# Kernel tuning notes

Measured on AMD Instinct MI355X. Metric: run time of the kernel, lower is better.

Reference implementation:

```python
import jax, jax.numpy as jnp
import numpy as np

HEADS = 16

def setup_inputs() -> dict:
    key = jax.random.key(0)
    k0, k1, k2, k3 = jax.random.split(key, 4)
    B, L, D = 2, 2048, 2048
    q = jax.random.normal(k0, (B, L, D), dtype=jnp.float32)
    k = jax.random.normal(k1, (B, L, D), dtype=jnp.float32)
    v = jax.random.normal(k2, (B, L, D), dtype=jnp.float32)
    wo = jax.random.normal(k3, (D, D), dtype=jnp.float32) * (1.0 / np.sqrt(D))
    return {"q": q, "k": k, "v": v, "wo": wo}

def reference(q, k, v, wo):
    B, Lq, D = q.shape
    Lk = k.shape[1]
    H = HEADS
    hd = D // H
    # [B, L, D] -> [B, H, L, hd]
    qh = q.reshape(B, Lq, H, hd).transpose(0, 2, 1, 3)
    kh = k.reshape(B, Lk, H, hd).transpose(0, 2, 1, 3)
    vh = v.reshape(B, Lk, H, hd).transpose(0, 2, 1, 3)
    scale = 1.0 / np.sqrt(hd).astype(np.float32)
    scores = jnp.einsum('bhqd,bhkd->bhqk', qh, kh) * scale
    cache_len = Lk - Lq
    # additive causal mask: -10000 above diagonal offset cache_len+1
    mask = jnp.triu(jnp.full((Lq, Lk), -10000.0, dtype=scores.dtype), k=cache_len + 1)
    attn = jax.nn.softmax(scores + mask, axis=-1)  # dropout p=0.0 => identity
    out = jnp.einsum('bhqk,bhkd->bhqd', attn, vh)
    out = out.transpose(0, 2, 1, 3).reshape(B, Lq, D)
    out = out @ wo.T  # torch Linear: x @ W^T
    return (out, kh, vh)
```

## Files before the change

kernel.cpp:

```cpp
#include <hip/hip_runtime.h>


typedef __attribute__((ext_vector_type(8))) __bf16 bf16x8;
typedef __attribute__((ext_vector_type(4))) float f32x4;
typedef __attribute__((ext_vector_type(4))) unsigned int uint32x4;

__device__ __forceinline__ unsigned short f2bf(float f) {
  union { float f; unsigned int u; } v; v.f = f;
  return (unsigned short)((v.u + 0x7FFFu + ((v.u >> 16) & 1u)) >> 16);
}
__device__ __forceinline__ __bf16 tobf(float f) {
  unsigned short u = f2bf(f);
  __bf16 r;
  __builtin_memcpy(&r, &u, 2);
  return r;
}
__device__ __forceinline__ float bfval(unsigned short u) {
  return __builtin_bit_cast(float, ((unsigned int)u) << 16);
}
__device__ __forceinline__ f32x4 zero4() {
  f32x4 z = {0.0f, 0.0f, 0.0f, 0.0f};
  return z;
}
__device__ __forceinline__ void gld_lds16(const unsigned short* g, unsigned short* l) {
  __builtin_amdgcn_global_load_lds(
      (const __attribute__((address_space(1))) unsigned int*)g,
      (__attribute__((address_space(3))) unsigned int*)l, 16, 0, 0);
}

__global__ __launch_bounds__(256) void conv_k(const float* __restrict__ k,
                                              float* __restrict__ kh,
                                              unsigned short* __restrict__ kbf) {
  int t = blockIdx.x * 256 + threadIdx.x;
  int d4 = t & 31;
  int l  = (t >> 5) & 2047;
  int h  = (t >> 16) & 15;
  int b  = t >> 20;
  const float4 v = *(const float4*)(k + ((size_t)(b * 2048 + l)) * 2048 + h * 128 + d4 * 4);
  size_t dst = (size_t)t * 4;
  *(float4*)(kh + dst) = v;
  *(ushort4*)(kbf + dst) = make_ushort4(f2bf(v.x), f2bf(v.y), f2bf(v.z), f2bf(v.w));
}

__global__ __launch_bounds__(256) void conv_wo(const float* __restrict__ wo,
                                               unsigned short* __restrict__ wobf) {
  int t = blockIdx.x * 256 + threadIdx.x;
  size_t dst = (size_t)t * 4;
  const float4 v = *(const float4*)(wo + dst);
  *(ushort4*)(wobf + dst) = make_ushort4(f2bf(v.x), f2bf(v.y), f2bf(v.z), f2bf(v.w));
}

__global__ __launch_bounds__(256) void conv_v(const float* __restrict__ v,
                                              float* __restrict__ vh,
                                              unsigned short* __restrict__ vbt) {
  __shared__ __align__(16) unsigned short T[128 * 72];
  const int tid = threadIdx.x;
  const int bid = blockIdx.x;
  const int lt = bid & 31;
  const int h  = (bid >> 5) & 15;
  const int b  = bid >> 9;
  const int l0 = lt * 64;
  const int bh = b * 16 + h;
#pragma unroll
  for (int i = 0; i < 8; ++i) {
    int c = tid + 256 * i;
    int row = c >> 5, col4 = c & 31;
    const float4 x = *(const float4*)(v + ((size_t)(b * 2048 + l0 + row)) * 2048 + h * 128 + col4 * 4);
    *(float4*)(vh + ((size_t)(bh * 2048 + l0 + row)) * 128 + col4 * 4) = x;
    T[(col4 * 4 + 0) * 72 + row] = f2bf(x.x);
    T[(col4 * 4 + 1) * 72 + row] = f2bf(x.y);
    T[(col4 * 4 + 2) * 72 + row] = f2bf(x.z);
    T[(col4 * 4 + 3) * 72 + row] = f2bf(x.w);
  }
  __syncthreads();
#pragma unroll
  for (int i = 0; i < 4; ++i) {
    int c = tid + 256 * i;
    int dR = c >> 3, cIdx = c & 7;
    int s2 = cIdx >> 2, qd = cIdx & 3;
    const unsigned short* Tr = &T[dR * 72];
    uint4 o4;
    o4.x = *(const unsigned int*)&Tr[0 * 16 + qd * 4 + 2 * s2];
    o4.y = *(const unsigned int*)&Tr[1 * 16 + qd * 4 + 2 * s2];
    o4.z = *(const unsigned int*)&Tr[2 * 16 + qd * 4 + 2 * s2];
    o4.w = *(const unsigned int*)&Tr[3 * 16 + qd * 4 + 2 * s2];
    *(uint4*)(vbt + ((size_t)(bh * 128 + dR)) * 2048 + l0 + cIdx * 8) = o4;
  }
}

__global__ __launch_bounds__(256) void flash_attn(const float* __restrict__ q,
                                                  const unsigned short* __restrict__ kbf,
                                                  const unsigned short* __restrict__ vbt,
                                                  unsigned short* __restrict__ ctx) {
  __shared__ __align__(16) unsigned short K2[2][64 * 128];
  __shared__ __align__(16) unsigned short V2[2][128 * 64];
  const int tid = threadIdx.x;
  const int w = tid >> 6, lane = tid & 63;
  const int lo = lane & 15, quad = lane >> 4;
  const int bid = blockIdx.x;
  const int pair = bid & 15;
  const int bh = bid >> 4;
  const int b = bh >> 4, h = bh & 15;
  const unsigned short* kg0 = kbf + (size_t)bh * 2048 * 128;
  const unsigned short* vg0 = vbt + (size_t)bh * 128 * 2048;
  const float qscale = 0.08838834764831845f * 1.4426950408889634f;

  auto stage = [&](int buf, int k0) {
#pragma unroll
    for (int i = 0; i < 4; ++i) {
      int c = tid + 256 * i;
      int row = c >> 4, p = c & 15;
      int g = (p & 8) | ((p & 7) ^ (row & 7));
      gld_lds16(kg0 + (size_t)(k0 + row) * 128 + g * 8, &K2[buf][(w * 64 + 256 * i) * 8]);
    }
#pragma unroll
    for (int i = 0; i < 4; ++i) {
      int c = tid + 256 * i;
      int row = c >> 3, p = c & 7;
      int g = p ^ (row & 7);
      gld_lds16(vg0 + (size_t)row * 2048 + k0 + g * 8, &V2[buf][(w * 64 + 256 * i) * 8]);
    }
  };

  for (int phase = 0; phase < 2; ++phase) {
    const int qt = phase ? 31 - pair : pair;
    const int q0 = qt * 64;
    const int qrow = q0 + w * 16 + lo;

    stage(0, 0);

    bf16x8 qf[4];
    {
      const float* qb = q + ((size_t)(b * 2048 + q0 + w * 16 + lo)) * 2048 + h * 128;
#pragma unroll
      for (int kb = 0; kb < 4; ++kb) {
        float4 x = *(const float4*)(qb + kb * 32 + quad * 8);
        float4 y = *(const float4*)(qb + kb * 32 + quad * 8 + 4);
        bf16x8 f;
        f[0] = tobf(x.x * qscale); f[1] = tobf(x.y * qscale);
        f[2] = tobf(x.z * qscale); f[3] = tobf(x.w * qscale);
        f[4] = tobf(y.x * qscale); f[5] = tobf(y.y * qscale);
        f[6] = tobf(y.z * qscale); f[7] = tobf(y.w * qscale);
        qf[kb] = f;
      }
    }

    f32x4 o[8];
#pragma unroll
    for (int i = 0; i < 8; ++i) o[i] = zero4();
    float lsum = 0.0f;

    for (int kt = 0; kt <= qt; ++kt) {
      __syncthreads();
      if (kt < qt) stage((kt + 1) & 1, (kt + 1) * 64);
      const int buf = kt & 1;
      const int k0 = kt * 64;

      f32x4 s[4];
#pragma unroll
      for (int nb = 0; nb < 4; ++nb) {
        f32x4 z = zero4();
#pragma unroll
        for (int kb = 0; kb < 4; ++kb) {
          int row = nb * 16 + lo;
          int g = kb * 4 + quad;
          int p = (g & 8) | ((g & 7) ^ (row & 7));
          bf16x8 kf = *(const bf16x8*)&K2[buf][row * 128 + p * 8];
          z = __builtin_amdgcn_mfma_f32_16x16x32_bf16(kf, qf[kb], z, 0, 0, 0);
        }
        s[nb] = z;
      }

      if (kt == qt) {
#pragma unroll
        for (int nb = 0; nb < 4; ++nb) {
          int keyb = k0 + nb * 16 + quad * 4;
#pragma unroll
          for (int r = 0; r < 4; ++r) {
            if (keyb + r > qrow) s[nb][r] = -1e30f;
          }
        }
      }

      unsigned int pk[4][2];
#pragma unroll
      for (int nb = 0; nb < 4; ++nb) {
#pragma unroll
        for (int s2 = 0; s2 < 2; ++s2) {
          float p0 = __builtin_amdgcn_exp2f(s[nb][2 * s2]);
          float p1 = __builtin_amdgcn_exp2f(s[nb][2 * s2 + 1]);
          unsigned short u0 = f2bf(p0);
          unsigned short u1 = f2bf(p1);
          pk[nb][s2] = (unsigned int)u0 | ((unsigned int)u1 << 16);
          lsum += bfval(u0);
          lsum += bfval(u1);
        }
      }

      bf16x8 pa[2];
#pragma unroll
      for (int kb2 = 0; kb2 < 2; ++kb2) {
        uint32x4 t;
        t[0] = pk[0][kb2]; t[1] = pk[1][kb2]; t[2] = pk[2][kb2]; t[3] = pk[3][kb2];
        pa[kb2] = __builtin_bit_cast(bf16x8, t);
      }

#pragma unroll
      for (int ob = 0; ob < 8; ++ob) {
#pragma unroll
        for (int kb2 = 0; kb2 < 2; ++kb2) {
          int row = ob * 16 + lo;
          int g = kb2 * 4 + quad;
          int p = g ^ (row & 7);
          bf16x8 vf = *(const bf16x8*)&V2[buf][row * 64 + p * 8];
          o[ob] = __builtin_amdgcn_mfma_f32_16x16x32_bf16(vf, pa[kb2], o[ob], 0, 0, 0);
        }
      }
    }
    __syncthreads();

    lsum += __shfl_xor(lsum, 16);
    lsum += __shfl_xor(lsum, 32);
    const float linv = 1.0f / lsum;

    unsigned short* cb = ctx + ((size_t)(b * 2048 + q0 + w * 16 + lo)) * 2048 + h * 128 + quad * 4;
#pragma unroll
    for (int ob = 0; ob < 8; ++ob) {
      ushort4 pkk = make_ushort4(f2bf(o[ob][0] * linv), f2bf(o[ob][1] * linv),
                                 f2bf(o[ob][2] * linv), f2bf(o[ob][3] * linv));
      *(ushort4*)(cb + ob * 16) = pkk;
    }
  }
}

__global__ __launch_bounds__(256) void gemm_bt(const unsigned short* __restrict__ A,
                                               const unsigned short* __restrict__ Bm,
                                               float* __restrict__ C) {
  __shared__ __align__(16) unsigned short As[2][128 * 64];
  __shared__ __align__(16) unsigned short Bs[2][128 * 64];
  const int tid = threadIdx.x;
  const int w = tid >> 6, lane = tid & 63;
  const int lo = lane & 15, quad = lane >> 4;
  const int nbid = blockIdx.x & 15;
  const int mbid = blockIdx.x >> 4;
  const int m0 = mbid * 128, n0 = nbid * 128;
  const int wr = w >> 1, wc = w & 1;

  auto stage = [&](int buf, int k0) {
#pragma unroll
    for (int i = 0; i < 4; ++i) {
      int c = tid + 256 * i;
      int row = c >> 3, p = c & 7;
      int g = p ^ (row & 7);
      gld_lds16(A + (size_t)(m0 + row) * 2048 + k0 + g * 8, &As[buf][(w * 64 + 256 * i) * 8]);
    }
#pragma unroll
    for (int i = 0; i < 4; ++i) {
      int c = tid + 256 * i;
      int row = c >> 3, p = c & 7;
      int g = p ^ (row & 7);
      gld_lds16(Bm + (size_t)(n0 + row) * 2048 + k0 + g * 8, &Bs[buf][(w * 64 + 256 * i) * 8]);
    }
  };

  f32x4 acc[4][4];
#pragma unroll
  for (int i = 0; i < 4; ++i)
#pragma unroll
    for (int j = 0; j < 4; ++j) acc[i][j] = zero4();

  stage(0, 0);
  for (int kt = 0; kt < 32; ++kt) {
    __syncthreads();
    if (kt < 31) stage((kt + 1) & 1, (kt + 1) * 64);
    const int buf = kt & 1;
#pragma unroll
    for (int kb = 0; kb < 2; ++kb) {
      bf16x8 af[4], bfr[4];
#pragma unroll
      for (int mi = 0; mi < 4; ++mi) {
        int row = wr * 64 + mi * 16 + lo;
        int g = kb * 4 + quad;
        int p = g ^ (row & 7);
        af[mi] = *(const bf16x8*)&As[buf][row * 64 + p * 8];
      }
#pragma unroll
      for (int ni = 0; ni < 4; ++ni) {
        int row = wc * 64 + ni * 16 + lo;
        int g = kb * 4 + quad;
        int p = g ^ (row & 7);
        bfr[ni] = *(const bf16x8*)&Bs[buf][row * 64 + p * 8];
      }
#pragma unroll
      for (int mi = 0; mi < 4; ++mi)
#pragma unroll
        for (int ni = 0; ni < 4; ++ni)
          acc[mi][ni] = __builtin_amdgcn_mfma_f32_16x16x32_bf16(af[mi], bfr[ni], acc[mi][ni], 0, 0, 0);
    }
  }
#pragma unroll
  for (int mi = 0; mi < 4; ++mi)
#pragma unroll
    for (int ni = 0; ni < 4; ++ni)
#pragma unroll
      for (int r = 0; r < 4; ++r) {
        int row = m0 + wr * 64 + mi * 16 + quad * 4 + r;
        int col = n0 + wc * 64 + ni * 16 + lo;
        C[(size_t)row * 2048 + col] = acc[mi][ni][r];
      }
}

extern "C" void kernel_launch(void* const* d_in, const int* in_sizes, int n_in,
                              void* d_out, int out_size, void* d_ws, size_t ws_size,
                              hipStream_t stream) {
  const float* q  = (const float*)d_in[0];
  const float* k  = (const float*)d_in[1];
  const float* v  = (const float*)d_in[2];
  const float* wo = (const float*)d_in[3];

  float* outp = (float*)d_out;
  float* kh   = outp + 8388608;
  float* vh   = outp + 16777216;

  unsigned short* ws   = (unsigned short*)d_ws;
  unsigned short* kbf  = ws;
  unsigned short* vbt  = kbf + 8388608;
  unsigned short* wobf = vbt + 8388608;
  unsigned short* ctx  = wobf + 4194304;

  conv_k<<<8192, 256, 0, stream>>>(k, kh, kbf);
  conv_v<<<1024, 256, 0, stream>>>(v, vh, vbt);
  conv_wo<<<4096, 256, 0, stream>>>(wo, wobf);
  flash_attn<<<512, 256, 0, stream>>>(q, kbf, vbt, ctx);
  gemm_bt<<<512, 256, 0, stream>>>(ctx, wobf, outp);
}
```

Baseline: 316.2 us.

## Use 128-row query tiles with 8 waves sharing each staged K/V tile

The flash attention kernel now uses 512-thread blocks covering 128 query rows, so each staged 64-key K/V tile is shared by twice as many waves. Grid size halves to 256 blocks. Waves whose rows lie entirely before a key tile skip its compute, and masking applies only to the last two tiles. Bf16 conversions switch to native casts, and the row sum now adds unrounded fp32 probabilities instead of the bf16-rounded ones fed to the MFMA. Fewer blocks may underfill the GPU and cause more tail imbalance.

Result: faster. 301.7 us (-4.6%).

```diff
diff --git a/kernel.cpp b/kernel.cpp
--- a/kernel.cpp
+++ b/kernel.cpp
@@ -2,21 +2,12 @@
 
 
 typedef __attribute__((ext_vector_type(8))) __bf16 bf16x8;
+typedef __attribute__((ext_vector_type(4))) __bf16 bf16x4;
 typedef __attribute__((ext_vector_type(4))) float f32x4;
-typedef __attribute__((ext_vector_type(4))) unsigned int uint32x4;
 
 __device__ __forceinline__ unsigned short f2bf(float f) {
   union { float f; unsigned int u; } v; v.f = f;
   return (unsigned short)((v.u + 0x7FFFu + ((v.u >> 16) & 1u)) >> 16);
-}
-__device__ __forceinline__ __bf16 tobf(float f) {
-  unsigned short u = f2bf(f);
-  __bf16 r;
-  __builtin_memcpy(&r, &u, 2);
-  return r;
-}
-__device__ __forceinline__ float bfval(unsigned short u) {
-  return __builtin_bit_cast(float, ((unsigned int)u) << 16);
 }
 __device__ __forceinline__ f32x4 zero4() {
   f32x4 z = {0.0f, 0.0f, 0.0f, 0.0f};
@@ -88,7 +79,7 @@
   }
 }
 
-__global__ __launch_bounds__(256) void flash_attn(const float* __restrict__ q,
+__global__ __launch_bounds__(512) void flash_attn(const float* __restrict__ q,
                                                   const unsigned short* __restrict__ kbf,
                                                   const unsigned short* __restrict__ vbt,
                                                   unsigned short* __restrict__ ctx) {
@@ -98,8 +89,8 @@
   const int w = tid >> 6, lane = tid & 63;
   const int lo = lane & 15, quad = lane >> 4;
   const int bid = blockIdx.x;
-  const int pair = bid & 15;
-  const int bh = bid >> 4;
+  const int pair = bid & 7;
+  const int bh = bid >> 3;
   const int b = bh >> 4, h = bh & 15;
   const unsigned short* kg0 = kbf + (size_t)bh * 2048 * 128;
   const unsigned short* vg0 = vbt + (size_t)bh * 128 * 2048;
@@ -107,25 +98,26 @@
 
   auto stage = [&](int buf, int k0) {
 #pragma unroll
-    for (int i = 0; i < 4; ++i) {
-      int c = tid + 256 * i;
+    for (int i = 0; i < 2; ++i) {
+      int c = tid + 512 * i;
       int row = c >> 4, p = c & 15;
       int g = (p & 8) | ((p & 7) ^ (row & 7));
-      gld_lds16(kg0 + (size_t)(k0 + row) * 128 + g * 8, &K2[buf][(w * 64 + 256 * i) * 8]);
-    }
-#pragma unroll
-    for (int i = 0; i < 4; ++i) {
-      int c = tid + 256 * i;
+      gld_lds16(kg0 + (size_t)(k0 + row) * 128 + g * 8, &K2[buf][(w * 64 + 512 * i) * 8]);
+    }
+#pragma unroll
+    for (int i = 0; i < 2; ++i) {
+      int c = tid + 512 * i;
       int row = c >> 3, p = c & 7;
       int g = p ^ (row & 7);
-      gld_lds16(vg0 + (size_t)row * 2048 + k0 + g * 8, &V2[buf][(w * 64 + 256 * i) * 8]);
+      gld_lds16(vg0 + (size_t)row * 2048 + k0 + g * 8, &V2[buf][(w * 64 + 512 * i) * 8]);
     }
   };
 
   for (int phase = 0; phase < 2; ++phase) {
-    const int qt = phase ? 31 - pair : pair;
-    const int q0 = qt * 64;
+    const int qt = phase ? 15 - pair : pair;
+    const int q0 = qt * 128;
     const int qrow = q0 + w * 16 + lo;
+    const int ktlim = 2 * qt + 2;
 
     stage(0, 0);
 
@@ -137,10 +129,10 @@
         float4 x = *(const float4*)(qb + kb * 32 + quad * 8);
         float4 y = *(const float4*)(qb + kb * 32 + quad * 8 + 4);
         bf16x8 f;
-        f[0] = tobf(x.x * qscale); f[1] = tobf(x.y * qscale);
-        f[2] = tobf(x.z * qscale); f[3] = tobf(x.w * qscale);
-        f[4] = tobf(y.x * qscale); f[5] = tobf(y.y * qscale);
-        f[6] = tobf(y.z * qscale); f[7] = tobf(y.w * qscale);
+        f[0] = (__bf16)(x.x * qscale); f[1] = (__bf16)(x.y * qscale);
+        f[2] = (__bf16)(x.z * qscale); f[3] = (__bf16)(x.w * qscale);
+        f[4] = (__bf16)(y.x * qscale); f[5] = (__bf16)(y.y * qscale);
+        f[6] = (__bf16)(y.z * qscale); f[7] = (__bf16)(y.w * qscale);
         qf[kb] = f;
       }
     }
@@ -150,70 +142,62 @@
     for (int i = 0; i < 8; ++i) o[i] = zero4();
     float lsum = 0.0f;
 
-    for (int kt = 0; kt <= qt; ++kt) {
+    for (int kt = 0; kt < ktlim; ++kt) {
       __syncthreads();
-      if (kt < qt) stage((kt + 1) & 1, (kt + 1) * 64);
+      if (kt + 1 < ktlim) stage((kt + 1) & 1, (kt + 1) * 64);
       const int buf = kt & 1;
       const int k0 = kt * 64;
 
-      f32x4 s[4];
-#pragma unroll
-      for (int nb = 0; nb < 4; ++nb) {
-        f32x4 z = zero4();
-#pragma unroll
-        for (int kb = 0; kb < 4; ++kb) {
-          int row = nb * 16 + lo;
-          int g = kb * 4 + quad;
-          int p = (g & 8) | ((g & 7) ^ (row & 7));
-          bf16x8 kf = *(const bf16x8*)&K2[buf][row * 128 + p * 8];
-          z = __builtin_amdgcn_mfma_f32_16x16x32_bf16(kf, qf[kb], z, 0, 0, 0);
+      if (k0 <= q0 + w * 16 + 15) {
+        f32x4 s[4];
+#pragma unroll
+        for (int nb = 0; nb < 4; ++nb) {
+          f32x4 z = zero4();
+#pragma unroll
+          for (int kb = 0; kb < 4; ++kb) {
+            int row = nb * 16 + lo;
+            int g = kb * 4 + quad;
+            int p = (g & 8) | ((g & 7) ^ (row & 7));
+            bf16x8 kf = *(const bf16x8*)&K2[buf][row * 128 + p * 8];
+            z = __builtin_amdgcn_mfma_f32_16x16x32_bf16(kf, qf[kb], z, 0, 0, 0);
+          }
+          s[nb] = z;
         }
-        s[nb] = z;
-      }
-
-      if (kt == qt) {
-#pragma unroll
-        for (int nb = 0; nb < 4; ++nb) {
-          int keyb = k0 + nb * 16 + quad * 4;
-#pragma unroll
-          for (int r = 0; r < 4; ++r) {
-            if (keyb + r > qrow) s[nb][r] = -1e30f;
+
+        if (kt >= 2 * qt) {
+#pragma unroll
+          for (int nb = 0; nb < 4; ++nb) {
+            int keyb = k0 + nb * 16 + quad * 4;
+#pragma unroll
+            for (int r = 0; r < 4; ++r) {
+              if (keyb + r > qrow) s[nb][r] = -1e30f;
+            }
           }
         }
-      }
-
-      unsigned int pk[4][2];
-#pragma unroll
-      for (int nb = 0; nb < 4; ++nb) {
-#pragma unroll
-        for (int s2 = 0; s2 < 2; ++s2) {
-          float p0 = __builtin_amdgcn_exp2f(s[nb][2 * s2]);
-          float p1 = __builtin_amdgcn_exp2f(s[nb][2 * s2 + 1]);
-          unsigned short u0 = f2bf(p0);
-          unsigned short u1 = f2bf(p1);
-          pk[nb][s2] = (unsigned int)u0 | ((unsigned int)u1 << 16);
-          lsum += bfval(u0);
-          lsum += bfval(u1);
+
+        bf16x8 pa[2];
+#pragma unroll
+        for (int nb = 0; nb < 4; ++nb) {
+#pragma unroll
+          for (int s2 = 0; s2 < 2; ++s2) {
+            float p0 = __builtin_amdgcn_exp2f(s[nb][2 * s2]);
+            float p1 = __builtin_amdgcn_exp2f(s[nb][2 * s2 + 1]);
+            lsum += p0 + p1;
+            pa[s2][2 * nb]     = (__bf16)p0;
+            pa[s2][2 * nb + 1] = (__bf16)p1;
+          }
         }
-      }
-
-      bf16x8 pa[2];
-#pragma unroll
-      for (int kb2 = 0; kb2 < 2; ++kb2) {
-        uint32x4 t;
-        t[0] = pk[0][kb2]; t[1] = pk[1][kb2]; t[2] = pk[2][kb2]; t[3] = pk[3][kb2];
-        pa[kb2] = __builtin_bit_cast(bf16x8, t);
-      }
-
-#pragma unroll
-      for (int ob = 0; ob < 8; ++ob) {
-#pragma unroll
-        for (int kb2 = 0; kb2 < 2; ++kb2) {
-          int row = ob * 16 + lo;
-          int g = kb2 * 4 + quad;
-          int p = g ^ (row & 7);
-          bf16x8 vf = *(const bf16x8*)&V2[buf][row * 64 + p * 8];
-          o[ob] = __builtin_amdgcn_mfma_f32_16x16x32_bf16(vf, pa[kb2], o[ob], 0, 0, 0);
+
+#pragma unroll
+        for (int ob = 0; ob < 8; ++ob) {
+#pragma unroll
+          for (int kb2 = 0; kb2 < 2; ++kb2) {
+            int row = ob * 16 + lo;
+            int g = kb2 * 4 + quad;
+            int p = g ^ (row & 7);
+            bf16x8 vf = *(const bf16x8*)&V2[buf][row * 64 + p * 8];
+            o[ob] = __builtin_amdgcn_mfma_f32_16x16x32_bf16(vf, pa[kb2], o[ob], 0, 0, 0);
+          }
         }
       }
     }
@@ -226,9 +210,12 @@
     unsigned short* cb = ctx + ((size_t)(b * 2048 + q0 + w * 16 + lo)) * 2048 + h * 128 + quad * 4;
 #pragma unroll
     for (int ob = 0; ob < 8; ++ob) {
-      ushort4 pkk = make_ushort4(f2bf(o[ob][0] * linv), f2bf(o[ob][1] * linv),
-                                 f2bf(o[ob][2] * linv), f2bf(o[ob][3] * linv));
-      *(ushort4*)(cb + ob * 16) = pkk;
+      bf16x4 pk4;
+      pk4[0] = (__bf16)(o[ob][0] * linv);
+      pk4[1] = (__bf16)(o[ob][1] * linv);
+      pk4[2] = (__bf16)(o[ob][2] * linv);
+      pk4[3] = (__bf16)(o[ob][3] * linv);
+      *(bf16x4*)(cb + ob * 16) = pk4;
     }
   }
 }
@@ -331,6 +318,6 @@
   conv_k<<<8192, 256, 0, stream>>>(k, kh, kbf);
   conv_v<<<1024, 256, 0, stream>>>(v, vh, vbt);
   conv_wo<<<4096, 256, 0, stream>>>(wo, wobf);
-  flash_attn<<<512, 256, 0, stream>>>(q, kbf, vbt, ctx);
+  flash_attn<<<256, 512, 0, stream>>>(q, kbf, vbt, ctx);
   gemm_bt<<<512, 256, 0, stream>>>(ctx, wobf, outp);
 }
```
